# Optimization experiments

Measured on AMD Instinct MI355X. Metric: run time of the kernel, lower is better.

Reference implementation:

```python
import jax, jax.numpy as jnp
import numpy as np

B_BATCH, H_DIM, W_DIM, D_MODEL, N_STATE = 4, 64, 64, 512, 8


def setup_inputs() -> dict:
    key = jax.random.key(0)
    ks = jax.random.split(key, 7)
    x = jax.random.normal(ks[0], (B_BATCH, H_DIM * W_DIM, D_MODEL), jnp.float32)
    # stable diagonal recurrence: 0 < A < 1
    A = jax.random.uniform(ks[1], (D_MODEL, N_STATE), jnp.float32, 0.5, 0.99)
    Bm = jax.random.normal(ks[2], (D_MODEL, N_STATE), jnp.float32) * 0.1
    Cm = jax.random.normal(ks[3], (D_MODEL, N_STATE), jnp.float32) * 0.1
    D_skip = jax.random.normal(ks[4], (D_MODEL,), jnp.float32)
    Wp = jax.random.normal(ks[5], (D_MODEL, D_MODEL), jnp.float32) / np.sqrt(D_MODEL)
    b_proj = jnp.zeros((D_MODEL,), jnp.float32)
    return {"x": x, "h": H_DIM, "w": W_DIM, "A": A, "Bm": Bm, "Cm": Cm,
            "D_skip": D_skip, "Wp": Wp, "b_proj": b_proj}


def _ssm(xs, A, Bm, Cm, D_skip):
    # xs: (batch', L, d). Diagonal SSM: s_t = A*s_{t-1} + B*x_t; y_t = C.s_t + D*x_t
    bt, L, d = xs.shape
    n = A.shape[1]

    def step(s, x_t):  # s: (bt, d, n), x_t: (bt, d)
        s = A * s + Bm * x_t[:, :, None]
        y = jnp.einsum('bdn,dn->bd', s, Cm) + D_skip * x_t
        return s, y

    s0 = jnp.zeros((bt, d, n), xs.dtype)
    _, ys = jax.lax.scan(step, s0, jnp.swapaxes(xs, 0, 1))  # ys: (L, bt, d)
    return jnp.swapaxes(ys, 0, 1)


def reference(x, h, w, A, Bm, Cm, D_skip, Wp, b_proj):
    b, l, d = x.shape
    xg = x.reshape(b, h, w, d)
    # horizontal direction: 'b (h w) d -> (b w) h d' -> scan over h
    x_h = jnp.transpose(xg, (0, 2, 1, 3)).reshape(b * w, h, d)
    y_h = _ssm(x_h, A, Bm, Cm, D_skip).reshape(b, w, h, d)
    y_h = jnp.transpose(y_h, (0, 2, 1, 3)).reshape(b, l, d)
    # vertical direction: 'b (h w) d -> (b h) w d' -> scan over w
    x_v = xg.reshape(b * h, w, d)
    y_v = _ssm(x_v, A, Bm, Cm, D_skip).reshape(b, l, d)
    # fused add + output projection (Linear: x @ W.T + b)
    return (y_h + y_v) @ Wp.T + b_proj
```

## Files before the change

### kernel.cpp

```cpp
#include <hip/hip_runtime.h>

#define BB 4
#define HH 64
#define WW 64
#define DD 512
#define NS 8
#define MROWS (BB * HH * WW)

typedef __attribute__((ext_vector_type(8))) __bf16 bf16x8;
typedef __attribute__((ext_vector_type(4))) float f32x4;

__device__ inline short f2bf(float f) {
  unsigned u = __float_as_uint(f);
  return (short)((u + 0x7fff + ((u >> 16) & 1)) >> 16);
}
__device__ inline float bf2f(short s) {
  return __uint_as_float(((unsigned)(unsigned short)s) << 16);
}

__device__ inline float ssm_step(float xv, float* s, const float* a,
                                 const float* bm, const float* cm, float dk) {
#pragma unroll
  for (int n = 0; n < NS; ++n) s[n] = fmaf(a[n], s[n], bm[n] * xv);
  float p0 = s[0] * cm[0], p1 = s[1] * cm[1], p2 = s[2] * cm[2],
        p3 = s[3] * cm[3], p4 = s[4] * cm[4], p5 = s[5] * cm[5],
        p6 = s[6] * cm[6], p7 = s[7] * cm[7];
  float q0 = p0 + p1, q1 = p2 + p3, q2 = p4 + p5, q3 = p6 + p7;
  return fmaf(dk, xv, (q0 + q1) + (q2 + q3));
}

__global__ __launch_bounds__(256) void scan_h_kernel(
    const float* __restrict__ x, const float* __restrict__ A,
    const float* __restrict__ Bm, const float* __restrict__ Cm,
    const float* __restrict__ Dsk, short* __restrict__ y,
    const float* __restrict__ Wp, short* __restrict__ wb) {
  if (blockIdx.x >= 256) {
    const int cid = (blockIdx.x - 256) * 2 + blockIdx.y;
    const int i = (cid * 256 + (int)threadIdx.x) * 8;
    const float4 v0 = *(const float4*)&Wp[i];
    const float4 v1 = *(const float4*)&Wp[i + 4];
    short r[8];
    r[0] = f2bf(v0.x); r[1] = f2bf(v0.y); r[2] = f2bf(v0.z); r[3] = f2bf(v0.w);
    r[4] = f2bf(v1.x); r[5] = f2bf(v1.y); r[6] = f2bf(v1.z); r[7] = f2bf(v1.w);
    *(short4*)&wb[i] = *(short4*)&r[0];
    *(short4*)&wb[i + 4] = *(short4*)&r[4];
    return;
  }

  const int seq = blockIdx.x;
  const int d = blockIdx.y * 256 + threadIdx.x;
  const int b = seq >> 6;
  const int r = seq & 63;

  size_t base = ((size_t)b * HH * WW + r) * DD + d;
  const size_t step = (size_t)WW * DD;

  float a[NS], bm[NS], cm[NS], s[NS];
#pragma unroll
  for (int i = 0; i < NS; i += 4) {
    float4 t;
    t = *(const float4*)&A[(size_t)d * NS + i];
    a[i] = t.x; a[i + 1] = t.y; a[i + 2] = t.z; a[i + 3] = t.w;
    t = *(const float4*)&Bm[(size_t)d * NS + i];
    bm[i] = t.x; bm[i + 1] = t.y; bm[i + 2] = t.z; bm[i + 3] = t.w;
    t = *(const float4*)&Cm[(size_t)d * NS + i];
    cm[i] = t.x; cm[i + 1] = t.y; cm[i + 2] = t.z; cm[i + 3] = t.w;
  }
  const float dk = Dsk[d];
#pragma unroll
  for (int i = 0; i < NS; ++i) s[i] = 0.f;

  float xs[4][8];
#pragma unroll
  for (int i = 0; i < 8; ++i) xs[0][i] = x[base + (size_t)i * step];
#pragma unroll
  for (int i = 0; i < 8; ++i) xs[1][i] = x[base + (size_t)(8 + i) * step];

#pragma unroll 4
  for (int c = 0; c < 8; ++c) {
    const int cur = c & 3;
    if (c < 6) {
      const size_t pbase = base + 16 * step;
#pragma unroll
      for (int i = 0; i < 8; ++i)
        xs[(c + 2) & 3][i] = x[pbase + (size_t)i * step];
    }
#pragma unroll
    for (int i = 0; i < 8; ++i)
      y[base + (size_t)i * step] = f2bf(ssm_step(xs[cur][i], s, a, bm, cm, dk));
    base += 8 * step;
  }
}

__global__ __launch_bounds__(512) void scanv_gemm_kernel(
    const float* __restrict__ x, const float* __restrict__ A,
    const float* __restrict__ Bm, const float* __restrict__ Cm,
    const float* __restrict__ Dsk, const short* __restrict__ yh,
    const short* __restrict__ Wb, const float* __restrict__ bias,
    float* __restrict__ out) {
  __shared__ __align__(16) short Ys[64 * DD];
  __shared__ __align__(16) short Bs[2][DD * 32];

  const int tid = (int)threadIdx.x;
  const int lane = tid & 63;
  const int wid = tid >> 6;
  const int m0 = blockIdx.x * 64;
  const int d = tid;

  auto stageB = [&](int ks, int buf) {
    const int k0 = ks * 32;
#pragma unroll
    for (int c = 0; c < 4; ++c) {
      const int chunk = wid * 4 + c;
      const int n = chunk * 16 + (lane >> 2);
      const int kslot = ((lane & 3) ^ (n & 3)) << 3;
      const short* g = &Wb[(size_t)n * DD + k0 + kslot];
      __builtin_amdgcn_global_load_lds(
          (const __attribute__((address_space(1))) unsigned int*)g,
          (__attribute__((address_space(3))) unsigned int*)((char*)&Bs[buf][0] +
                                                            chunk * 1024),
          16, 0, 0);
    }
  };

  float a[NS], bm[NS], cm[NS], s[NS];
#pragma unroll
  for (int i = 0; i < NS; i += 4) {
    float4 t;
    t = *(const float4*)&A[(size_t)d * NS + i];
    a[i] = t.x; a[i + 1] = t.y; a[i + 2] = t.z; a[i + 3] = t.w;
    t = *(const float4*)&Bm[(size_t)d * NS + i];
    bm[i] = t.x; bm[i + 1] = t.y; bm[i + 2] = t.z; bm[i + 3] = t.w;
    t = *(const float4*)&Cm[(size_t)d * NS + i];
    cm[i] = t.x; cm[i + 1] = t.y; cm[i + 2] = t.z; cm[i + 3] = t.w;
  }
  const float dk = Dsk[d];
#pragma unroll
  for (int i = 0; i < NS; ++i) s[i] = 0.f;

  size_t base = (size_t)m0 * DD + d;
  stageB(0, 0);

  float xs[4][8], yp[4][8];
#pragma unroll
  for (int i = 0; i < 8; ++i) xs[0][i] = x[base + (size_t)i * DD];
#pragma unroll
  for (int i = 0; i < 8; ++i) yp[0][i] = bf2f(yh[base + (size_t)i * DD]);
#pragma unroll
  for (int i = 0; i < 8; ++i) xs[1][i] = x[base + (size_t)(8 + i) * DD];
#pragma unroll
  for (int i = 0; i < 8; ++i) yp[1][i] = bf2f(yh[base + (size_t)(8 + i) * DD]);

#pragma unroll 4
  for (int c = 0; c < 8; ++c) {
    const int cur = c & 3;
    if (c < 6) {
      const size_t pbase = base + 16 * DD;
#pragma unroll
      for (int i = 0; i < 8; ++i)
        xs[(c + 2) & 3][i] = x[pbase + (size_t)i * DD];
#pragma unroll
      for (int i = 0; i < 8; ++i)
        yp[(c + 2) & 3][i] = bf2f(yh[pbase + (size_t)i * DD]);
    }
#pragma unroll
    for (int i = 0; i < 8; ++i) {
      const int w = c * 8 + i;
      const float acc =
          ssm_step(xs[cur][i], s, a, bm, cm, dk) + yp[cur][i];
      Ys[w * DD + (d ^ ((w & 7) << 3))] = f2bf(acc);
    }
    base += 8 * DD;
  }

  __syncthreads();

  f32x4 acc4[4][4];
#pragma unroll
  for (int m = 0; m < 4; ++m)
#pragma unroll
    for (int n = 0; n < 4; ++n) acc4[m][n] = (f32x4){0.f, 0.f, 0.f, 0.f};

  const int fr = lane & 15;
  const int kfr = (lane >> 4) * 8;

  int cur = 0;
  for (int ks = 0; ks < 16; ++ks) {
    if (ks < 15) {
      stageB(ks + 1, cur ^ 1);
      asm volatile("s_waitcnt vmcnt(4)" ::: "memory");
    } else {
      asm volatile("s_waitcnt vmcnt(0)" ::: "memory");
    }
    __builtin_amdgcn_sched_barrier(0);

    bf16x8 af[4], bfv[4];
    const int kg = ks * 32 + kfr;
#pragma unroll
    for (int m = 0; m < 4; ++m) {
      const int r = m * 16 + fr;
      af[m] = *(const bf16x8*)(const void*)&Ys[r * DD + (kg ^ ((r & 7) << 3))];
    }
#pragma unroll
    for (int n = 0; n < 4; ++n) {
      const int nn = wid * 64 + n * 16 + fr;
      bfv[n] = *(const bf16x8*)(const void*)&Bs[cur][nn * 32 +
                                                     (kfr ^ ((nn & 3) << 3))];
    }
#pragma unroll
    for (int m = 0; m < 4; ++m)
#pragma unroll
      for (int n = 0; n < 4; ++n)
        acc4[m][n] = __builtin_amdgcn_mfma_f32_16x16x32_bf16(
            af[m], bfv[n], acc4[m][n], 0, 0, 0);
    __builtin_amdgcn_sched_barrier(0);
    cur ^= 1;
  }

  const int c16 = lane & 15;
  const int r4 = (lane >> 4) * 4;
#pragma unroll
  for (int m = 0; m < 4; ++m) {
    const int rowb = m0 + m * 16 + r4;
#pragma unroll
    for (int n = 0; n < 4; ++n) {
      const int col = wid * 64 + n * 16 + c16;
      const float bv = bias[col];
#pragma unroll
      for (int j = 0; j < 4; ++j)
        out[(size_t)(rowb + j) * DD + col] = acc4[m][n][j] + bv;
    }
  }
}

extern "C" void kernel_launch(void* const* d_in, const int* in_sizes, int n_in,
                              void* d_out, int out_size, void* d_ws,
                              size_t ws_size, hipStream_t stream) {
  const float* x = (const float*)d_in[0];
  const float* A = (const float*)d_in[3];
  const float* Bm = (const float*)d_in[4];
  const float* Cm = (const float*)d_in[5];
  const float* Dsk = (const float*)d_in[6];
  const float* Wp = (const float*)d_in[7];
  const float* bpj = (const float*)d_in[8];
  float* out = (float*)d_out;

  short* yh = (short*)d_ws;
  short* wb = (short*)((char*)d_ws + (size_t)MROWS * DD * 2);

  const dim3 grid_h(256 + 64, DD / 256);
  scan_h_kernel<<<grid_h, 256, 0, stream>>>(x, A, Bm, Cm, Dsk, yh, Wp, wb);

  scanv_gemm_kernel<<<BB * HH, 512, 0, stream>>>(x, A, Bm, Cm, Dsk, yh, wb,
                                                 bpj, out);
}
```

Before: 42.24 us.

## Interleave vertical scan with per-chunk GEMM and read weights directly from global

The vertical-scan kernel no longer finishes the whole 64-row scan before starting the projection GEMM. It now scans 16 rows, synchronises, and runs that row tile's MFMA GEMM before scanning the next 16, so scan latency can overlap with matrix work across waves. The LDS double buffer for the bf16 weight matrix is removed, and B fragments are loaded straight from global memory. This halves shared-memory use, but the block now re-reads the full weight matrix once per 16-row tile, which raises L2 traffic and load latency inside the GEMM loop.

```diff
diff --git a/kernel.cpp b/kernel.cpp
--- a/kernel.cpp
+++ b/kernel.cpp
@@ -99,29 +99,12 @@
     const short* __restrict__ Wb, const float* __restrict__ bias,
     float* __restrict__ out) {
   __shared__ __align__(16) short Ys[64 * DD];
-  __shared__ __align__(16) short Bs[2][DD * 32];
 
   const int tid = (int)threadIdx.x;
   const int lane = tid & 63;
   const int wid = tid >> 6;
   const int m0 = blockIdx.x * 64;
   const int d = tid;
-
-  auto stageB = [&](int ks, int buf) {
-    const int k0 = ks * 32;
-#pragma unroll
-    for (int c = 0; c < 4; ++c) {
-      const int chunk = wid * 4 + c;
-      const int n = chunk * 16 + (lane >> 2);
-      const int kslot = ((lane & 3) ^ (n & 3)) << 3;
-      const short* g = &Wb[(size_t)n * DD + k0 + kslot];
-      __builtin_amdgcn_global_load_lds(
-          (const __attribute__((address_space(1))) unsigned int*)g,
-          (__attribute__((address_space(3))) unsigned int*)((char*)&Bs[buf][0] +
-                                                            chunk * 1024),
-          16, 0, 0);
-    }
-  };
 
   float a[NS], bm[NS], cm[NS], s[NS];
 #pragma unroll
@@ -138,97 +121,82 @@
 #pragma unroll
   for (int i = 0; i < NS; ++i) s[i] = 0.f;
 
-  size_t base = (size_t)m0 * DD + d;
-  stageB(0, 0);
-
-  float xs[4][8], yp[4][8];
-#pragma unroll
-  for (int i = 0; i < 8; ++i) xs[0][i] = x[base + (size_t)i * DD];
-#pragma unroll
-  for (int i = 0; i < 8; ++i) yp[0][i] = bf2f(yh[base + (size_t)i * DD]);
-#pragma unroll
-  for (int i = 0; i < 8; ++i) xs[1][i] = x[base + (size_t)(8 + i) * DD];
-#pragma unroll
-  for (int i = 0; i < 8; ++i) yp[1][i] = bf2f(yh[base + (size_t)(8 + i) * DD]);
-
-#pragma unroll 4
-  for (int c = 0; c < 8; ++c) {
-    const int cur = c & 3;
-    if (c < 6) {
-      const size_t pbase = base + 16 * DD;
-#pragma unroll
-      for (int i = 0; i < 8; ++i)
-        xs[(c + 2) & 3][i] = x[pbase + (size_t)i * DD];
-#pragma unroll
-      for (int i = 0; i < 8; ++i)
-        yp[(c + 2) & 3][i] = bf2f(yh[pbase + (size_t)i * DD]);
-    }
-#pragma unroll
-    for (int i = 0; i < 8; ++i) {
-      const int w = c * 8 + i;
-      const float acc =
-          ssm_step(xs[cur][i], s, a, bm, cm, dk) + yp[cur][i];
-      Ys[w * DD + (d ^ ((w & 7) << 3))] = f2bf(acc);
-    }
-    base += 8 * DD;
-  }
-
-  __syncthreads();
-
-  f32x4 acc4[4][4];
-#pragma unroll
-  for (int m = 0; m < 4; ++m)
-#pragma unroll
-    for (int n = 0; n < 4; ++n) acc4[m][n] = (f32x4){0.f, 0.f, 0.f, 0.f};
-
   const int fr = lane & 15;
   const int kfr = (lane >> 4) * 8;
-
-  int cur = 0;
-  for (int ks = 0; ks < 16; ++ks) {
-    if (ks < 15) {
-      stageB(ks + 1, cur ^ 1);
-      asm volatile("s_waitcnt vmcnt(4)" ::: "memory");
-    } else {
-      asm volatile("s_waitcnt vmcnt(0)" ::: "memory");
-    }
-    __builtin_amdgcn_sched_barrier(0);
-
-    bf16x8 af[4], bfv[4];
-    const int kg = ks * 32 + kfr;
-#pragma unroll
-    for (int m = 0; m < 4; ++m) {
-      const int r = m * 16 + fr;
-      af[m] = *(const bf16x8*)(const void*)&Ys[r * DD + (kg ^ ((r & 7) << 3))];
-    }
-#pragma unroll
-    for (int n = 0; n < 4; ++n) {
-      const int nn = wid * 64 + n * 16 + fr;
-      bfv[n] = *(const bf16x8*)(const void*)&Bs[cur][nn * 32 +
-                                                     (kfr ^ ((nn & 3) << 3))];
-    }
-#pragma unroll
-    for (int m = 0; m < 4; ++m)
-#pragma unroll
-      for (int n = 0; n < 4; ++n)
-        acc4[m][n] = __builtin_amdgcn_mfma_f32_16x16x32_bf16(
-            af[m], bfv[n], acc4[m][n], 0, 0, 0);
-    __builtin_amdgcn_sched_barrier(0);
-    cur ^= 1;
-  }
-
   const int c16 = lane & 15;
   const int r4 = (lane >> 4) * 4;
+
+  float bv[4];
+#pragma unroll
+  for (int n = 0; n < 4; ++n) bv[n] = bias[wid * 64 + n * 16 + c16];
+
+  size_t base = (size_t)m0 * DD + d;
+
+  float xs[4][8], yp[4][8];
+#pragma unroll
+  for (int i = 0; i < 8; ++i) xs[0][i] = x[base + (size_t)i * DD];
+#pragma unroll
+  for (int i = 0; i < 8; ++i) yp[0][i] = bf2f(yh[base + (size_t)i * DD]);
+#pragma unroll
+  for (int i = 0; i < 8; ++i) xs[1][i] = x[base + (size_t)(8 + i) * DD];
+#pragma unroll
+  for (int i = 0; i < 8; ++i) yp[1][i] = bf2f(yh[base + (size_t)(8 + i) * DD]);
+
 #pragma unroll
   for (int m = 0; m < 4; ++m) {
+#pragma unroll
+    for (int cc = 0; cc < 2; ++cc) {
+      const int c = 2 * m + cc;
+      const int cur = c & 3;
+      if (c < 6) {
+        const size_t pbase = base + 16 * DD;
+#pragma unroll
+        for (int i = 0; i < 8; ++i)
+          xs[(c + 2) & 3][i] = x[pbase + (size_t)i * DD];
+#pragma unroll
+        for (int i = 0; i < 8; ++i)
+          yp[(c + 2) & 3][i] = bf2f(yh[pbase + (size_t)i * DD]);
+      }
+#pragma unroll
+      for (int i = 0; i < 8; ++i) {
+        const int w = c * 8 + i;
+        const float acc = ssm_step(xs[cur][i], s, a, bm, cm, dk) + yp[cur][i];
+        Ys[w * DD + (d ^ ((w & 7) << 3))] = f2bf(acc);
+      }
+      base += 8 * DD;
+    }
+
+    __syncthreads();
+
+    f32x4 acc4[4];
+#pragma unroll
+    for (int n = 0; n < 4; ++n) acc4[n] = (f32x4){0.f, 0.f, 0.f, 0.f};
+
+    const int r = m * 16 + fr;
+#pragma unroll 2
+    for (int ks = 0; ks < 16; ++ks) {
+      const int kg = ks * 32 + kfr;
+      const bf16x8 af =
+          *(const bf16x8*)(const void*)&Ys[r * DD + (kg ^ ((r & 7) << 3))];
+      bf16x8 bfv[4];
+#pragma unroll
+      for (int n = 0; n < 4; ++n) {
+        const int nn = wid * 64 + n * 16 + fr;
+        bfv[n] = *(const bf16x8*)(const void*)&Wb[(size_t)nn * DD + kg];
+      }
+#pragma unroll
+      for (int n = 0; n < 4; ++n)
+        acc4[n] =
+            __builtin_amdgcn_mfma_f32_16x16x32_bf16(af, bfv[n], acc4[n], 0, 0, 0);
+    }
+
     const int rowb = m0 + m * 16 + r4;
 #pragma unroll
     for (int n = 0; n < 4; ++n) {
       const int col = wid * 64 + n * 16 + c16;
-      const float bv = bias[col];
 #pragma unroll
       for (int j = 0; j < 4; ++j)
-        out[(size_t)(rowb + j) * DD + col] = acc4[m][n][j] + bv;
+        out[(size_t)(rowb + j) * DD + col] = acc4[n][j] + bv[n];
     }
   }
 }
```

After: 85.88 us. 2.03x slower.

## Chunk the horizontal scan into four segments with carry combine and fixup

Applied to the files above, without the earlier changes.

The horizontal scan is split into four 16-step chunks per sequence, so four times as many blocks run in parallel. Each chunk writes its final state as bf16 carries, and a new combine kernel propagates the carries across chunks. The vertical-scan/GEMM kernel then adds the correction C·A^(t+1)·carry per row when it loads yh. This shortens the serial dependency chain of the h-scan. In exchange it adds a third launch, extra carry traffic, a per-thread power loop, and bf16 rounding of the carry states.

```diff
diff --git a/kernel.cpp b/kernel.cpp
--- a/kernel.cpp
+++ b/kernel.cpp
@@ -6,6 +6,8 @@
 #define DD 512
 #define NS 8
 #define MROWS (BB * HH * WW)
+#define CL 16
+#define NCH 4
 
 typedef __attribute__((ext_vector_type(8))) __bf16 bf16x8;
 typedef __attribute__((ext_vector_type(4))) float f32x4;
@@ -16,6 +18,12 @@
 }
 __device__ inline float bf2f(short s) {
   return __uint_as_float(((unsigned)(unsigned short)s) << 16);
+}
+__device__ inline float bflo(unsigned u) {
+  return __uint_as_float(u << 16);
+}
+__device__ inline float bfhi(unsigned u) {
+  return __uint_as_float(u & 0xffff0000u);
 }
 
 __device__ inline float ssm_step(float xv, float* s, const float* a,
@@ -29,14 +37,16 @@
   return fmaf(dk, xv, (q0 + q1) + (q2 + q3));
 }
 
-__global__ __launch_bounds__(256) void scan_h_kernel(
+__global__ __launch_bounds__(512, 6) void scan_h_chunked(
     const float* __restrict__ x, const float* __restrict__ A,
     const float* __restrict__ Bm, const float* __restrict__ Cm,
-    const float* __restrict__ Dsk, short* __restrict__ y,
-    const float* __restrict__ Wp, short* __restrict__ wb) {
-  if (blockIdx.x >= 256) {
-    const int cid = (blockIdx.x - 256) * 2 + blockIdx.y;
-    const int i = (cid * 256 + (int)threadIdx.x) * 8;
+    const float* __restrict__ Dsk, short* __restrict__ yh,
+    short* __restrict__ c16, const float* __restrict__ Wp,
+    short* __restrict__ wb) {
+  const int bx = (int)blockIdx.x;
+  const int tid = (int)threadIdx.x;
+  if (bx >= 1024) {
+    const int i = ((bx - 1024) * 512 + tid) * 8;
     const float4 v0 = *(const float4*)&Wp[i];
     const float4 v1 = *(const float4*)&Wp[i + 4];
     short r[8];
@@ -47,13 +57,11 @@
     return;
   }
 
-  const int seq = blockIdx.x;
-  const int d = blockIdx.y * 256 + threadIdx.x;
+  const int seq = bx >> 2;
+  const int ch = bx & 3;
   const int b = seq >> 6;
-  const int r = seq & 63;
-
-  size_t base = ((size_t)b * HH * WW + r) * DD + d;
-  const size_t step = (size_t)WW * DD;
+  const int w = seq & 63;
+  const int d = tid;
 
   float a[NS], bm[NS], cm[NS], s[NS];
 #pragma unroll
@@ -70,25 +78,63 @@
 #pragma unroll
   for (int i = 0; i < NS; ++i) s[i] = 0.f;
 
-  float xs[4][8];
-#pragma unroll
-  for (int i = 0; i < 8; ++i) xs[0][i] = x[base + (size_t)i * step];
-#pragma unroll
-  for (int i = 0; i < 8; ++i) xs[1][i] = x[base + (size_t)(8 + i) * step];
-
-#pragma unroll 4
-  for (int c = 0; c < 8; ++c) {
-    const int cur = c & 3;
-    if (c < 6) {
-      const size_t pbase = base + 16 * step;
-#pragma unroll
-      for (int i = 0; i < 8; ++i)
-        xs[(c + 2) & 3][i] = x[pbase + (size_t)i * step];
-    }
-#pragma unroll
-    for (int i = 0; i < 8; ++i)
-      y[base + (size_t)i * step] = f2bf(ssm_step(xs[cur][i], s, a, bm, cm, dk));
-    base += 8 * step;
+  const size_t step = (size_t)WW * DD;
+  size_t base = ((size_t)b * HH * WW + (size_t)(ch * CL) * WW + w) * DD + d;
+
+  float xv[CL];
+#pragma unroll
+  for (int i = 0; i < CL; ++i) xv[i] = x[base + (size_t)i * step];
+
+#pragma unroll
+  for (int i = 0; i < CL; ++i)
+    yh[base + (size_t)i * step] = f2bf(ssm_step(xv[i], s, a, bm, cm, dk));
+
+  if (ch < 3) {
+    short r[8];
+#pragma unroll
+    for (int n = 0; n < NS; ++n) r[n] = f2bf(s[n]);
+    const size_t cb = (((size_t)seq * 3 + ch) * DD + d) * 8;
+    *(short4*)&c16[cb] = *(short4*)&r[0];
+    *(short4*)&c16[cb + 4] = *(short4*)&r[4];
+  }
+}
+
+__global__ __launch_bounds__(512) void combine_carries(
+    const float* __restrict__ A, const short* __restrict__ c16,
+    short* __restrict__ E) {
+  const int seq = (int)blockIdx.x;
+  const int d = (int)threadIdx.x;
+
+  float a[NS];
+  const float4 t0 = *(const float4*)&A[(size_t)d * NS];
+  const float4 t1 = *(const float4*)&A[(size_t)d * NS + 4];
+  a[0] = t0.x; a[1] = t0.y; a[2] = t0.z; a[3] = t0.w;
+  a[4] = t1.x; a[5] = t1.y; a[6] = t1.z; a[7] = t1.w;
+  float p16[NS];
+#pragma unroll
+  for (int n = 0; n < NS; ++n) p16[n] = a[n];
+#pragma unroll
+  for (int q = 0; q < 4; ++q)
+#pragma unroll
+    for (int n = 0; n < NS; ++n) p16[n] *= p16[n];
+
+  const size_t rb = ((size_t)seq * 3) * DD * 8 + (size_t)d * 8;
+  float e[NS];
+#pragma unroll
+  for (int n = 0; n < NS; ++n) e[n] = 0.f;
+#pragma unroll
+  for (int j = 0; j < 3; ++j) {
+    const uint4 u = *(const uint4*)&c16[rb + (size_t)j * DD * 8];
+    float c[NS];
+    c[0] = bflo(u.x); c[1] = bfhi(u.x); c[2] = bflo(u.y); c[3] = bfhi(u.y);
+    c[4] = bflo(u.z); c[5] = bfhi(u.z); c[6] = bflo(u.w); c[7] = bfhi(u.w);
+#pragma unroll
+    for (int n = 0; n < NS; ++n) e[n] = fmaf(p16[n], e[n], c[n]);
+    short r[8];
+#pragma unroll
+    for (int n = 0; n < NS; ++n) r[n] = f2bf(e[n]);
+    *(short4*)&E[rb + (size_t)j * DD * 8] = *(short4*)&r[0];
+    *(short4*)&E[rb + (size_t)j * DD * 8 + 4] = *(short4*)&r[4];
   }
 }
 
@@ -96,8 +142,8 @@
     const float* __restrict__ x, const float* __restrict__ A,
     const float* __restrict__ Bm, const float* __restrict__ Cm,
     const float* __restrict__ Dsk, const short* __restrict__ yh,
-    const short* __restrict__ Wb, const float* __restrict__ bias,
-    float* __restrict__ out) {
+    const short* __restrict__ E, const short* __restrict__ Wb,
+    const float* __restrict__ bias, float* __restrict__ out) {
   __shared__ __align__(16) short Ys[64 * DD];
   __shared__ __align__(16) short Bs[2][DD * 32];
 
@@ -106,6 +152,10 @@
   const int wid = tid >> 6;
   const int m0 = blockIdx.x * 64;
   const int d = tid;
+  const int b = (int)blockIdx.x >> 6;
+  const int h = (int)blockIdx.x & 63;
+  const int ch = h >> 4;
+  const int tl = h & 15;
 
   auto stageB = [&](int ks, int buf) {
     const int k0 = ks * 32;
@@ -138,6 +188,33 @@
 #pragma unroll
   for (int i = 0; i < NS; ++i) s[i] = 0.f;
 
+  float coef[NS];
+  {
+    float ap[NS];
+#pragma unroll
+    for (int n = 0; n < NS; ++n) ap[n] = a[n];
+    for (int t = 0; t < tl; ++t)
+#pragma unroll
+      for (int n = 0; n < NS; ++n) ap[n] *= a[n];
+#pragma unroll
+    for (int n = 0; n < NS; ++n) coef[n] = cm[n] * ap[n];
+  }
+  const size_t e0 =
+      (ch > 0) ? (((size_t)(b * 64) * 3 + (ch - 1)) * DD + d) * 8 : 0;
+
+  auto ld_yp = [&](size_t ybase, int w) -> float {
+    float v = bf2f(yh[ybase]);
+    if (ch > 0) {
+      const uint4 eu = *(const uint4*)&E[e0 + (size_t)w * (3 * DD * 8)];
+      float t0 = fmaf(coef[0], bflo(eu.x), coef[1] * bfhi(eu.x));
+      float t1 = fmaf(coef[2], bflo(eu.y), coef[3] * bfhi(eu.y));
+      float t2 = fmaf(coef[4], bflo(eu.z), coef[5] * bfhi(eu.z));
+      float t3 = fmaf(coef[6], bflo(eu.w), coef[7] * bfhi(eu.w));
+      v += (t0 + t1) + (t2 + t3);
+    }
+    return v;
+  };
+
   size_t base = (size_t)m0 * DD + d;
   stageB(0, 0);
 
@@ -145,11 +222,12 @@
 #pragma unroll
   for (int i = 0; i < 8; ++i) xs[0][i] = x[base + (size_t)i * DD];
 #pragma unroll
-  for (int i = 0; i < 8; ++i) yp[0][i] = bf2f(yh[base + (size_t)i * DD]);
+  for (int i = 0; i < 8; ++i) yp[0][i] = ld_yp(base + (size_t)i * DD, i);
 #pragma unroll
   for (int i = 0; i < 8; ++i) xs[1][i] = x[base + (size_t)(8 + i) * DD];
 #pragma unroll
-  for (int i = 0; i < 8; ++i) yp[1][i] = bf2f(yh[base + (size_t)(8 + i) * DD]);
+  for (int i = 0; i < 8; ++i)
+    yp[1][i] = ld_yp(base + (size_t)(8 + i) * DD, 8 + i);
 
 #pragma unroll 4
   for (int c = 0; c < 8; ++c) {
@@ -161,13 +239,12 @@
         xs[(c + 2) & 3][i] = x[pbase + (size_t)i * DD];
 #pragma unroll
       for (int i = 0; i < 8; ++i)
-        yp[(c + 2) & 3][i] = bf2f(yh[pbase + (size_t)i * DD]);
+        yp[(c + 2) & 3][i] = ld_yp(pbase + (size_t)i * DD, (c + 2) * 8 + i);
     }
 #pragma unroll
     for (int i = 0; i < 8; ++i) {
       const int w = c * 8 + i;
-      const float acc =
-          ssm_step(xs[cur][i], s, a, bm, cm, dk) + yp[cur][i];
+      const float acc = ssm_step(xs[cur][i], s, a, bm, cm, dk) + yp[cur][i];
       Ys[w * DD + (d ^ ((w & 7) << 3))] = f2bf(acc);
     }
     base += 8 * DD;
@@ -217,14 +294,14 @@
     cur ^= 1;
   }
 
-  const int c16 = lane & 15;
+  const int c16l = lane & 15;
   const int r4 = (lane >> 4) * 4;
 #pragma unroll
   for (int m = 0; m < 4; ++m) {
     const int rowb = m0 + m * 16 + r4;
 #pragma unroll
     for (int n = 0; n < 4; ++n) {
-      const int col = wid * 64 + n * 16 + c16;
+      const int col = wid * 64 + n * 16 + c16l;
       const float bv = bias[col];
 #pragma unroll
       for (int j = 0; j < 4; ++j)
@@ -245,12 +322,15 @@
   const float* bpj = (const float*)d_in[8];
   float* out = (float*)d_out;
 
-  short* yh = (short*)d_ws;
-  short* wb = (short*)((char*)d_ws + (size_t)MROWS * DD * 2);
-
-  const dim3 grid_h(256 + 64, DD / 256);
-  scan_h_kernel<<<grid_h, 256, 0, stream>>>(x, A, Bm, Cm, Dsk, yh, Wp, wb);
-
-  scanv_gemm_kernel<<<BB * HH, 512, 0, stream>>>(x, A, Bm, Cm, Dsk, yh, wb,
+  char* ws = (char*)d_ws;
+  short* yh = (short*)ws;
+  short* wb = (short*)(ws + 16u * 1024 * 1024);
+  short* c16 = (short*)(ws + 17u * 1024 * 1024);
+  short* E = (short*)(ws + 24u * 1024 * 1024);
+
+  scan_h_chunked<<<1024 + 64, 512, 0, stream>>>(x, A, Bm, Cm, Dsk, yh, c16,
+                                                Wp, wb);
+  combine_carries<<<256, 512, 0, stream>>>(A, c16, E);
+  scanv_gemm_kernel<<<BB * HH, 512, 0, stream>>>(x, A, Bm, Cm, Dsk, yh, E, wb,
                                                  bpj, out);
 }
```

Result: slower. 77.41 us (+83.3%).

## Warp-specialize scan-v/GEMM kernel with producer-consumer flags to overlap scan and MFMA

Applied to the files above, without the earlier changes.

The fused vertical-scan plus projection kernel grows from 512 to 1024 threads. Eight waves run the vertical scan and publish each half of the 64-row tile through LDS atomic flags. The other eight waves run the GEMM on each 32-row half as soon as its flag is set. This overlaps scan latency with MFMA work and B-tile staging, but each GEMM wave now streams W twice (once per half), doubling global/LDS B traffic, and the larger block may limit occupancy and raise register pressure.

```diff
diff --git a/kernel.cpp b/kernel.cpp
--- a/kernel.cpp
+++ b/kernel.cpp
@@ -92,143 +92,171 @@
   }
 }
 
-__global__ __launch_bounds__(512) void scanv_gemm_kernel(
+__global__ __launch_bounds__(1024) void scanv_gemm_kernel(
     const float* __restrict__ x, const float* __restrict__ A,
     const float* __restrict__ Bm, const float* __restrict__ Cm,
     const float* __restrict__ Dsk, const short* __restrict__ yh,
     const short* __restrict__ Wb, const float* __restrict__ bias,
     float* __restrict__ out) {
-  __shared__ __align__(16) short Ys[64 * DD];
-  __shared__ __align__(16) short Bs[2][DD * 32];
+  __shared__ __align__(16) char LDSBUF[131072 + 16];
+  short* Ys = (short*)LDSBUF;
+  short* Bs0 = (short*)(LDSBUF + 65536);
+  short* Bs1 = (short*)(LDSBUF + 98304);
+  int* flags = (int*)(LDSBUF + 131072);
 
   const int tid = (int)threadIdx.x;
   const int lane = tid & 63;
   const int wid = tid >> 6;
   const int m0 = blockIdx.x * 64;
-  const int d = tid;
-
-  auto stageB = [&](int ks, int buf) {
-    const int k0 = ks * 32;
-#pragma unroll
-    for (int c = 0; c < 4; ++c) {
-      const int chunk = wid * 4 + c;
-      const int n = chunk * 16 + (lane >> 2);
-      const int kslot = ((lane & 3) ^ (n & 3)) << 3;
-      const short* g = &Wb[(size_t)n * DD + k0 + kslot];
-      __builtin_amdgcn_global_load_lds(
-          (const __attribute__((address_space(1))) unsigned int*)g,
-          (__attribute__((address_space(3))) unsigned int*)((char*)&Bs[buf][0] +
-                                                            chunk * 1024),
-          16, 0, 0);
-    }
-  };
-
-  float a[NS], bm[NS], cm[NS], s[NS];
-#pragma unroll
-  for (int i = 0; i < NS; i += 4) {
-    float4 t;
-    t = *(const float4*)&A[(size_t)d * NS + i];
-    a[i] = t.x; a[i + 1] = t.y; a[i + 2] = t.z; a[i + 3] = t.w;
-    t = *(const float4*)&Bm[(size_t)d * NS + i];
-    bm[i] = t.x; bm[i + 1] = t.y; bm[i + 2] = t.z; bm[i + 3] = t.w;
-    t = *(const float4*)&Cm[(size_t)d * NS + i];
-    cm[i] = t.x; cm[i + 1] = t.y; cm[i + 2] = t.z; cm[i + 3] = t.w;
-  }
-  const float dk = Dsk[d];
-#pragma unroll
-  for (int i = 0; i < NS; ++i) s[i] = 0.f;
-
-  size_t base = (size_t)m0 * DD + d;
-  stageB(0, 0);
-
-  float xs[4][8], yp[4][8];
-#pragma unroll
-  for (int i = 0; i < 8; ++i) xs[0][i] = x[base + (size_t)i * DD];
-#pragma unroll
-  for (int i = 0; i < 8; ++i) yp[0][i] = bf2f(yh[base + (size_t)i * DD]);
-#pragma unroll
-  for (int i = 0; i < 8; ++i) xs[1][i] = x[base + (size_t)(8 + i) * DD];
-#pragma unroll
-  for (int i = 0; i < 8; ++i) yp[1][i] = bf2f(yh[base + (size_t)(8 + i) * DD]);
+
+  if (tid < 2) flags[tid] = 0;
+  __syncthreads();
+
+  if (wid < 8) {
+    const int d = tid;
+    float a[NS], bm[NS], cm[NS], s[NS];
+#pragma unroll
+    for (int i = 0; i < NS; i += 4) {
+      float4 t;
+      t = *(const float4*)&A[(size_t)d * NS + i];
+      a[i] = t.x; a[i + 1] = t.y; a[i + 2] = t.z; a[i + 3] = t.w;
+      t = *(const float4*)&Bm[(size_t)d * NS + i];
+      bm[i] = t.x; bm[i + 1] = t.y; bm[i + 2] = t.z; bm[i + 3] = t.w;
+      t = *(const float4*)&Cm[(size_t)d * NS + i];
+      cm[i] = t.x; cm[i + 1] = t.y; cm[i + 2] = t.z; cm[i + 3] = t.w;
+    }
+    const float dk = Dsk[d];
+#pragma unroll
+    for (int i = 0; i < NS; ++i) s[i] = 0.f;
+
+    size_t base = (size_t)m0 * DD + d;
+    float xs[4][8], yp[4][8];
+#pragma unroll
+    for (int i = 0; i < 8; ++i) xs[0][i] = x[base + (size_t)i * DD];
+#pragma unroll
+    for (int i = 0; i < 8; ++i) yp[0][i] = bf2f(yh[base + (size_t)i * DD]);
+#pragma unroll
+    for (int i = 0; i < 8; ++i) xs[1][i] = x[base + (size_t)(8 + i) * DD];
+#pragma unroll
+    for (int i = 0; i < 8; ++i)
+      yp[1][i] = bf2f(yh[base + (size_t)(8 + i) * DD]);
 
 #pragma unroll 4
-  for (int c = 0; c < 8; ++c) {
-    const int cur = c & 3;
-    if (c < 6) {
-      const size_t pbase = base + 16 * DD;
-#pragma unroll
-      for (int i = 0; i < 8; ++i)
-        xs[(c + 2) & 3][i] = x[pbase + (size_t)i * DD];
-#pragma unroll
-      for (int i = 0; i < 8; ++i)
-        yp[(c + 2) & 3][i] = bf2f(yh[pbase + (size_t)i * DD]);
-    }
-#pragma unroll
-    for (int i = 0; i < 8; ++i) {
-      const int w = c * 8 + i;
-      const float acc =
-          ssm_step(xs[cur][i], s, a, bm, cm, dk) + yp[cur][i];
-      Ys[w * DD + (d ^ ((w & 7) << 3))] = f2bf(acc);
-    }
-    base += 8 * DD;
-  }
-
-  __syncthreads();
-
-  f32x4 acc4[4][4];
-#pragma unroll
-  for (int m = 0; m < 4; ++m)
-#pragma unroll
-    for (int n = 0; n < 4; ++n) acc4[m][n] = (f32x4){0.f, 0.f, 0.f, 0.f};
-
-  const int fr = lane & 15;
-  const int kfr = (lane >> 4) * 8;
-
-  int cur = 0;
-  for (int ks = 0; ks < 16; ++ks) {
-    if (ks < 15) {
-      stageB(ks + 1, cur ^ 1);
-      asm volatile("s_waitcnt vmcnt(4)" ::: "memory");
-    } else {
-      asm volatile("s_waitcnt vmcnt(0)" ::: "memory");
-    }
-    __builtin_amdgcn_sched_barrier(0);
-
-    bf16x8 af[4], bfv[4];
-    const int kg = ks * 32 + kfr;
+    for (int c = 0; c < 8; ++c) {
+      const int cur = c & 3;
+      if (c < 6) {
+        const size_t pbase = base + 16 * DD;
+#pragma unroll
+        for (int i = 0; i < 8; ++i)
+          xs[(c + 2) & 3][i] = x[pbase + (size_t)i * DD];
+#pragma unroll
+        for (int i = 0; i < 8; ++i)
+          yp[(c + 2) & 3][i] = bf2f(yh[pbase + (size_t)i * DD]);
+      }
+#pragma unroll
+      for (int i = 0; i < 8; ++i) {
+        const int w = c * 8 + i;
+        const float acc = ssm_step(xs[cur][i], s, a, bm, cm, dk) + yp[cur][i];
+        Ys[w * DD + (d ^ ((w & 7) << 3))] = f2bf(acc);
+      }
+      base += 8 * DD;
+      if (c == 3 || c == 7) {
+        asm volatile("s_waitcnt lgkmcnt(0)" ::: "memory");
+        if (lane == 0)
+          __hip_atomic_fetch_add(&flags[c >> 2], 1, __ATOMIC_RELEASE,
+                                 __HIP_MEMORY_SCOPE_WORKGROUP);
+      }
+    }
+  } else {
+    const int g = wid - 8;
+    const int fr = lane & 15;
+    const int kfr = (lane >> 4) * 8;
+
+    auto stageB = [&](int ks, short* bsb) {
+      const int k0 = ks * 32;
+#pragma unroll
+      for (int c = 0; c < 4; ++c) {
+        const int chunk = g * 4 + c;
+        const int n = chunk * 16 + (lane >> 2);
+        const int kslot = ((lane & 3) ^ (n & 3)) << 3;
+        const short* gp = &Wb[(size_t)n * DD + k0 + kslot];
+        __builtin_amdgcn_global_load_lds(
+            (const __attribute__((address_space(1))) unsigned int*)gp,
+            (__attribute__((address_space(3))) unsigned int*)((char*)bsb +
+                                                              chunk * 1024),
+            16, 0, 0);
+      }
+    };
+
+    f32x4 acc4[4][4];
+#pragma unroll
+    for (int m = 0; m < 4; ++m)
+#pragma unroll
+      for (int n = 0; n < 4; ++n) acc4[m][n] = (f32x4){0.f, 0.f, 0.f, 0.f};
+
+    stageB(0, Bs0);
+    int cur = 0;
+
+#pragma unroll
+    for (int p = 0; p < 2; ++p) {
+      while (__hip_atomic_load(&flags[p], __ATOMIC_ACQUIRE,
+                               __HIP_MEMORY_SCOPE_WORKGROUP) < 8)
+        __builtin_amdgcn_s_sleep(2);
+
+      for (int ks = 0; ks < 16; ++ks) {
+        const bool last = (p == 1) && (ks == 15);
+        if (!last) {
+          stageB((ks + 1) & 15, cur ? Bs0 : Bs1);
+          asm volatile("s_waitcnt vmcnt(4)" ::: "memory");
+        } else {
+          asm volatile("s_waitcnt vmcnt(0)" ::: "memory");
+        }
+        __builtin_amdgcn_sched_barrier(0);
+
+        const short* bsr = cur ? Bs1 : Bs0;
+        const int kg = ks * 32 + kfr;
+        bf16x8 a0, a1, bfv[4];
+        {
+          const int r0 = (2 * p) * 16 + fr;
+          const int r1 = (2 * p + 1) * 16 + fr;
+          a0 = *(const bf16x8*)(const void*)&Ys[r0 * DD +
+                                                (kg ^ ((r0 & 7) << 3))];
+          a1 = *(const bf16x8*)(const void*)&Ys[r1 * DD +
+                                                (kg ^ ((r1 & 7) << 3))];
+        }
+#pragma unroll
+        for (int n = 0; n < 4; ++n) {
+          const int nn = g * 64 + n * 16 + fr;
+          bfv[n] = *(const bf16x8*)(const void*)&bsr[nn * 32 +
+                                                     (kfr ^ ((nn & 3) << 3))];
+        }
+#pragma unroll
+        for (int n = 0; n < 4; ++n) {
+          acc4[2 * p][n] = __builtin_amdgcn_mfma_f32_16x16x32_bf16(
+              a0, bfv[n], acc4[2 * p][n], 0, 0, 0);
+          acc4[2 * p + 1][n] = __builtin_amdgcn_mfma_f32_16x16x32_bf16(
+              a1, bfv[n], acc4[2 * p + 1][n], 0, 0, 0);
+        }
+        __builtin_amdgcn_sched_barrier(0);
+        cur ^= 1;
+      }
+    }
+
+    const int c16 = lane & 15;
+    const int r4 = (lane >> 4) * 4;
+    float bv[4];
+#pragma unroll
+    for (int n = 0; n < 4; ++n) bv[n] = bias[g * 64 + n * 16 + c16];
 #pragma unroll
     for (int m = 0; m < 4; ++m) {
-      const int r = m * 16 + fr;
-      af[m] = *(const bf16x8*)(const void*)&Ys[r * DD + (kg ^ ((r & 7) << 3))];
-    }
-#pragma unroll
-    for (int n = 0; n < 4; ++n) {
-      const int nn = wid * 64 + n * 16 + fr;
-      bfv[n] = *(const bf16x8*)(const void*)&Bs[cur][nn * 32 +
-                                                     (kfr ^ ((nn & 3) << 3))];
-    }
-#pragma unroll
-    for (int m = 0; m < 4; ++m)
-#pragma unroll
-      for (int n = 0; n < 4; ++n)
-        acc4[m][n] = __builtin_amdgcn_mfma_f32_16x16x32_bf16(
-            af[m], bfv[n], acc4[m][n], 0, 0, 0);
-    __builtin_amdgcn_sched_barrier(0);
-    cur ^= 1;
-  }
-
-  const int c16 = lane & 15;
-  const int r4 = (lane >> 4) * 4;
-#pragma unroll
-  for (int m = 0; m < 4; ++m) {
-    const int rowb = m0 + m * 16 + r4;
-#pragma unroll
-    for (int n = 0; n < 4; ++n) {
-      const int col = wid * 64 + n * 16 + c16;
-      const float bv = bias[col];
-#pragma unroll
-      for (int j = 0; j < 4; ++j)
-        out[(size_t)(rowb + j) * DD + col] = acc4[m][n][j] + bv;
+      const int rowb = m0 + m * 16 + r4;
+#pragma unroll
+      for (int n = 0; n < 4; ++n) {
+        const int col = g * 64 + n * 16 + c16;
+#pragma unroll
+        for (int j = 0; j < 4; ++j)
+          out[(size_t)(rowb + j) * DD + col] = acc4[m][n][j] + bv[n];
+      }
     }
   }
 }
@@ -251,6 +279,6 @@
   const dim3 grid_h(256 + 64, DD / 256);
   scan_h_kernel<<<grid_h, 256, 0, stream>>>(x, A, Bm, Cm, Dsk, yh, Wp, wb);
 
-  scanv_gemm_kernel<<<BB * HH, 512, 0, stream>>>(x, A, Bm, Cm, Dsk, yh, wb,
-                                                 bpj, out);
-}
+  scanv_gemm_kernel<<<BB * HH, 1024, 0, stream>>>(x, A, Bm, Cm, Dsk, yh, wb,
+                                                  bpj, out);
+}
```

Result: slower. 58.07 us (+37.5%).
